# Optimization experiments

Hardware: AMD Instinct MI355X
Metric: run time of the kernel (lower is better)

Reference implementation:

```python
import jax, jax.numpy as jnp
import numpy as np

P = 2          # number of additive secret shares (2-party)
B = 2          # batch
S = 1024       # seq_len
D = 1024       # hidden_size
H = 16         # num_attention_heads
HD = D // H    # attention_head_size = 64
MASK_VAL = -10000.0


def setup_inputs() -> dict:
    key = jax.random.key(0)
    ks = jax.random.split(key, 6)
    w_scale = 0.02
    return {
        "hidden_shares": jax.random.normal(ks[0], (P, B, S, D), jnp.float32),
        "attention_mask": jnp.ones((B, S), jnp.float32),
        "wq": jax.random.normal(ks[1], (D, D), jnp.float32) * w_scale,
        "bq": jnp.zeros((D,), jnp.float32),
        "wk": jax.random.normal(ks[2], (D, D), jnp.float32) * w_scale,
        "bk": jnp.zeros((D,), jnp.float32),
        "wv": jax.random.normal(ks[3], (D, D), jnp.float32) * w_scale,
        "bv": jnp.zeros((D,), jnp.float32),
        "wo": jax.random.normal(ks[4], (D, D), jnp.float32) * w_scale,
        "bo": jnp.zeros((D,), jnp.float32),
    }


def reference(hidden_shares, attention_mask, wq, bq, wk, bk, wv, bv, wo, bo):
    """Secret-shared multi-head attention. Values are carried as P additive
    shares (leading axis); interactive protocol ops (matmul, softmax) are
    modeled as reconstruct -> compute -> reshare with fresh correlated masks,
    which is exactly the plaintext semantics the MPC protocol realizes."""
    scale = np.float32(1.0 / np.sqrt(HD))
    base = jax.random.key(42)  # protocol PRG for resharing masks

    def recon(x):  # [P, ...] -> [...]
        return x.sum(0)

    def reshare(v, tag):  # value -> P additive shares summing to v
        m = jax.random.normal(jax.random.fold_in(base, tag), v.shape, v.dtype) * 0.1
        return jnp.stack([v - m, m])

    def secure_linear(x_sh, w, b, tag):  # torch Linear: x @ w.T + b
        return reshare(recon(x_sh) @ w.T + b, tag)

    def split_heads(x_sh):  # [P,B,S,D] -> [P,B,H,S,HD] (per-share reshape/permute)
        return x_sh.reshape(P, B, S, H, HD).transpose(0, 1, 3, 2, 4)

    q = split_heads(secure_linear(hidden_shares, wq, bq, 0))
    k = split_heads(secure_linear(hidden_shares, wk, bk, 1))
    v = split_heads(secure_linear(hidden_shares, wv, bv, 2))

    # secure QK^T (matmul via reconstruct/reshare), then public scalar scale per-share
    scores = reshare(jnp.einsum('bhsd,bhtd->bhst', recon(q), recon(k)), 3) * scale

    # additive mask, shared, then share-wise secure_add
    additive = (1.0 - attention_mask)[:, None, None, :] * MASK_VAL  # [B,1,1,S]
    scores = scores + reshare(additive, 4)

    probs = reshare(jax.nn.softmax(recon(scores), axis=-1), 5)
    ctx = reshare(jnp.einsum('bhst,bhtd->bhsd', recon(probs), recon(v)), 6)

    # transpose back from scores: [P,B,H,S,HD] -> [P,B,S,D]
    ctx = ctx.transpose(0, 1, 3, 2, 4).reshape(P, B, S, D)

    out = secure_linear(ctx, wo, bo, 7)
    return recon(out)  # reconstructed output [B, S, D]
```

## Files before the change

kernel.cpp:

```cpp
#include <hip/hip_runtime.h>
#include <hip/hip_bf16.h>

#define BB 2
#define SS 1024
#define DD 1024
#define HH 16
#define HDD 64
#define MASK_VAL -10000.0f
#define LOG2E 1.44269504f
#define BSD (BB * SS * DD)
#define NROW (BB * HH * SS)
#define NKV 2

typedef __attribute__((ext_vector_type(8))) short bf16x8;
typedef __attribute__((ext_vector_type(4))) short short4v;
typedef __attribute__((ext_vector_type(4))) float f32x4;
typedef __attribute__((ext_vector_type(16))) float f32x16;
typedef __attribute__((ext_vector_type(4))) unsigned int uint4v;

__device__ __forceinline__ short f2bf(float f) {
    union { float f; unsigned u; } v; v.f = f;
    unsigned r = v.u + 0x7FFFu + ((v.u >> 16) & 1u);
    return (short)(r >> 16);
}
__device__ __forceinline__ float bf2f(short s) {
    union { unsigned u; float f; } v;
    v.u = ((unsigned)(unsigned short)s) << 16;
    return v.f;
}
__device__ __forceinline__ unsigned cvt_pk_bf16(float lo, float hi) {
    unsigned r;
    asm("v_cvt_pk_bf16_f32 %0, %1, %2" : "=v"(r) : "v"(lo), "v"(hi));
    return r;
}
__device__ __forceinline__ float v_exp2(float x) {
    float r;
    asm("v_exp_f32 %0, %1" : "=v"(r) : "v"(x));
    return r;
}
__device__ __forceinline__ void plane32_swap(unsigned& a, unsigned& b) {
#if __has_builtin(__builtin_amdgcn_permlane32_swap)
    auto r = __builtin_amdgcn_permlane32_swap(a, b, false, false);
    a = r[0]; b = r[1];
#else
    unsigned as = (unsigned)__shfl_xor((int)a, 32);
    unsigned bs = (unsigned)__shfl_xor((int)b, 32);
    bool lo = ((threadIdx.x & 63) < 32);
    unsigned na = lo ? a : bs;
    unsigned nb = lo ? as : b;
    a = na; b = nb;
#endif
}

__global__ __launch_bounds__(256) void k_prep(
    const float* __restrict__ h,
    const float* __restrict__ wq, const float* __restrict__ wk,
    const float* __restrict__ wv, const float* __restrict__ wo,
    short* __restrict__ xbf, short* __restrict__ wbf) {
    int id = blockIdx.x;
    if (id < 1024) {
        int i = id * 256 + threadIdx.x;
        const float4* h0 = (const float4*)h;
        const float4* h1 = (const float4*)(h + (size_t)BSD);
        float4 a0 = h0[2 * i], a1 = h0[2 * i + 1];
        float4 b0 = h1[2 * i], b1 = h1[2 * i + 1];
        bf16x8 o;
        o[0] = f2bf(a0.x + b0.x); o[1] = f2bf(a0.y + b0.y);
        o[2] = f2bf(a0.z + b0.z); o[3] = f2bf(a0.w + b0.w);
        o[4] = f2bf(a1.x + b1.x); o[5] = f2bf(a1.y + b1.y);
        o[6] = f2bf(a1.z + b1.z); o[7] = f2bf(a1.w + b1.w);
        ((bf16x8*)xbf)[i] = o;
    } else {
        int zi = (id - 1024) >> 9;
        int i = ((id - 1024) & 511) * 256 + threadIdx.x;
        const float* src = (zi == 0) ? wq : (zi == 1) ? wk : (zi == 2) ? wv : wo;
        short* dst = wbf + (size_t)zi * (DD * DD);
        const float4* s4 = (const float4*)src;
        float4 a0 = s4[2 * i], a1 = s4[2 * i + 1];
        bf16x8 o;
        o[0] = f2bf(a0.x); o[1] = f2bf(a0.y); o[2] = f2bf(a0.z); o[3] = f2bf(a0.w);
        o[4] = f2bf(a1.x); o[5] = f2bf(a1.y); o[6] = f2bf(a1.z); o[7] = f2bf(a1.w);
        ((bf16x8*)dst)[i] = o;
    }
}

#define QBM 128
#define QBN 64
#define QBK 64

__global__ __launch_bounds__(256) void k_gemm_qkv(
    const short* __restrict__ xbf, const short* __restrict__ wbf,
    const float* __restrict__ bq, const float* __restrict__ bk,
    const float* __restrict__ bv,
    short* __restrict__ qb, short* __restrict__ kb, short* __restrict__ vt) {
    __shared__ __align__(16) short As[QBM * QBK];
    __shared__ __align__(16) short Bs[QBN * QBK];
    const int z = blockIdx.z;
    const short* W = wbf + (size_t)z * (DD * DD);
    const float* bias = (z == 0) ? bq : (z == 1) ? bk : bv;
    const int bm = blockIdx.y * QBM;
    const int bn = blockIdx.x * QBN;
    const int tid = threadIdx.x;
    const int lane = tid & 63;
    const int wid = tid >> 6;
    const int wm = wid >> 1;
    const int wn = wid & 1;
    const int lr = lane & 15;
    const int kq = lane >> 4;

    f32x4 acc[4][2];
#pragma unroll
    for (int i = 0; i < 4; ++i)
#pragma unroll
        for (int j = 0; j < 2; ++j) acc[i][j] = (f32x4)0.0f;

    for (int k0 = 0; k0 < DD; k0 += QBK) {
#pragma unroll
        for (int i = 0; i < 4; ++i) {
            int s = i * 256 + tid;
            int r = s >> 3;
            int cs = (s & 7) ^ (r & 7);
            __builtin_amdgcn_global_load_lds(
                (const __attribute__((address_space(1))) unsigned*)(xbf + (size_t)(bm + r) * DD + k0 + (cs << 3)),
                (__attribute__((address_space(3))) unsigned*)&As[s * 8], 16, 0, 0);
        }
#pragma unroll
        for (int i = 0; i < 2; ++i) {
            int s = i * 256 + tid;
            int r = s >> 3;
            int cs = (s & 7) ^ (r & 7);
            __builtin_amdgcn_global_load_lds(
                (const __attribute__((address_space(1))) unsigned*)(W + (size_t)(bn + r) * DD + k0 + (cs << 3)),
                (__attribute__((address_space(3))) unsigned*)&Bs[s * 8], 16, 0, 0);
        }
        __syncthreads();

        bf16x8 af[4][2], bfr[2][2];
#pragma unroll
        for (int f = 0; f < 4; ++f) {
            int row = wm * 64 + f * 16 + lr;
#pragma unroll
            for (int ks = 0; ks < 2; ++ks) {
                int cpos = ((ks << 2) | kq) ^ (row & 7);
                af[f][ks] = *(const bf16x8*)&As[row * QBK + (cpos << 3)];
            }
        }
#pragma unroll
        for (int g = 0; g < 2; ++g) {
            int row = wn * 32 + g * 16 + lr;
#pragma unroll
            for (int ks = 0; ks < 2; ++ks) {
                int cpos = ((ks << 2) | kq) ^ (row & 7);
                bfr[g][ks] = *(const bf16x8*)&Bs[row * QBK + (cpos << 3)];
            }
        }
#pragma unroll
        for (int fm = 0; fm < 4; ++fm)
#pragma unroll
            for (int fn = 0; fn < 2; ++fn)
#pragma unroll
                for (int ks = 0; ks < 2; ++ks)
                    acc[fm][fn] = __builtin_amdgcn_mfma_f32_16x16x32_bf16(
                        af[fm][ks], bfr[fn][ks], acc[fm][fn], 0, 0, 0);
        __syncthreads();
    }

    if (z < 2) {
        short* C = (z == 0) ? qb : kb;
#pragma unroll
        for (int fm = 0; fm < 4; ++fm) {
            int row0 = bm + wm * 64 + fm * 16 + kq * 4;
#pragma unroll
            for (int fn = 0; fn < 2; ++fn) {
                int col = bn + wn * 32 + fn * 16 + lr;
                float bv_ = bias[col];
#pragma unroll
                for (int j = 0; j < 4; ++j)
                    C[(size_t)(row0 + j) * DD + col] = f2bf(acc[fm][fn][j] + bv_);
            }
        }
    } else {
#pragma unroll
        for (int fm = 0; fm < 4; ++fm) {
            int row0 = bm + wm * 64 + fm * 16 + kq * 4;
            int bidx = row0 >> 10, s0 = row0 & 1023;
#pragma unroll
            for (int fn = 0; fn < 2; ++fn) {
                int col = bn + wn * 32 + fn * 16 + lr;
                float bv_ = bias[col];
                size_t addr = ((size_t)(bidx * HH + (col >> 6)) * HDD + (col & 63)) * SS + s0;
                short4v o;
                o.x = f2bf(acc[fm][fn][0] + bv_); o.y = f2bf(acc[fm][fn][1] + bv_);
                o.z = f2bf(acc[fm][fn][2] + bv_); o.w = f2bf(acc[fm][fn][3] + bv_);
                *(short4v*)&vt[addr] = o;
            }
        }
    }
}

#define OM 64
#define ON 64
#define OK 64

__global__ __launch_bounds__(256) void k_gemm_out_fused(
    const short* __restrict__ Op, const float* __restrict__ Mp,
    const float* __restrict__ Lp, const short* __restrict__ W,
    const float* __restrict__ bias, float* __restrict__ C) {
    __shared__ __align__(16) short As[OM * OK];
    __shared__ __align__(16) short Bs[ON * OK];
    const int bm = blockIdx.y * OM;
    const int bn = blockIdx.x * ON;
    const int tid = threadIdx.x;
    const int lane = tid & 63;
    const int wid = tid >> 6;
    const int wm = wid & 1;
    const int wn = wid >> 1;
    const int lr = lane & 15;
    const int kq = lane >> 4;

    f32x4 acc[2][2];
#pragma unroll
    for (int i = 0; i < 2; ++i)
#pragma unroll
        for (int j = 0; j < 2; ++j) acc[i][j] = (f32x4)0.0f;

    for (int k0 = 0; k0 < DD; k0 += OK) {
#pragma unroll
        for (int i = 0; i < 2; ++i) {
            int t2 = i * 256 + tid;
            int br = t2 >> 3;
            int cs = (t2 & 7) ^ (br & 7);
            __builtin_amdgcn_global_load_lds(
                (const __attribute__((address_space(1))) unsigned*)(W + (size_t)(bn + br) * DD + k0 + (cs << 3)),
                (__attribute__((address_space(3))) unsigned*)&Bs[t2 * 8], 16, 0, 0);
        }
        int hh = k0 >> 6;
#pragma unroll
        for (int i = 0; i < 2; ++i) {
            int t2 = i * 256 + tid;
            int ar = t2 >> 3;
            int p = t2 & 7;
            int d0 = (p ^ (ar & 7)) << 3;
            int grow = bm + ar;
            int b = grow >> 10;
            int s = grow & 1023;
            int hrow = ((b * HH + hh) << 10) + s;
            float m1 = Mp[hrow], m2 = Mp[NROW + hrow];
            float l1 = Lp[hrow], l2 = Lp[NROW + hrow];
            float m = fmaxf(m1, m2);
            float a1 = v_exp2(m1 - m), a2 = v_exp2(m2 - m);
            float inv = 1.0f / (l1 * a1 + l2 * a2);
            float c1 = a1 * inv, c2 = a2 * inv;
            bf16x8 o1 = *(const bf16x8*)&Op[(size_t)hrow * HDD + d0];
            bf16x8 o2 = *(const bf16x8*)&Op[((size_t)NROW + hrow) * HDD + d0];
            bf16x8 av;
#pragma unroll
            for (int e = 0; e < 8; ++e)
                av[e] = f2bf(bf2f(o1[e]) * c1 + bf2f(o2[e]) * c2);
            *(bf16x8*)&As[t2 * 8] = av;
        }
        __syncthreads();

        bf16x8 af[2][2], bfr[2][2];
#pragma unroll
        for (int f = 0; f < 2; ++f) {
            int rowa = wm * 32 + f * 16 + lr;
            int rowb = wn * 32 + f * 16 + lr;
#pragma unroll
            for (int ks = 0; ks < 2; ++ks) {
                int ca = (((ks << 2) | kq)) ^ (rowa & 7);
                int cb = (((ks << 2) | kq)) ^ (rowb & 7);
                af[f][ks] = *(const bf16x8*)&As[rowa * OK + (ca << 3)];
                bfr[f][ks] = *(const bf16x8*)&Bs[rowb * OK + (cb << 3)];
            }
        }
#pragma unroll
        for (int fm = 0; fm < 2; ++fm)
#pragma unroll
            for (int fn = 0; fn < 2; ++fn)
#pragma unroll
                for (int ks = 0; ks < 2; ++ks)
                    acc[fm][fn] = __builtin_amdgcn_mfma_f32_16x16x32_bf16(
                        af[fm][ks], bfr[fn][ks], acc[fm][fn], 0, 0, 0);
        __syncthreads();
    }

#pragma unroll
    for (int fm = 0; fm < 2; ++fm) {
        int row0 = bm + wm * 32 + fm * 16 + kq * 4;
#pragma unroll
        for (int fn = 0; fn < 2; ++fn) {
            int col = bn + wn * 32 + fn * 16 + lr;
            float bv_ = bias[col];
#pragma unroll
            for (int j = 0; j < 4; ++j)
                C[(size_t)(row0 + j) * DD + col] = acc[fm][fn][j] + bv_;
        }
    }
}

__global__ __launch_bounds__(256) void k_attn(
    const short* __restrict__ qb, const short* __restrict__ kb,
    const short* __restrict__ vt, const float* __restrict__ mask,
    short* __restrict__ Op, float* __restrict__ Mp, float* __restrict__ Lp) {
    __shared__ __align__(16) short Kls[2][64 * 64];
    __shared__ __align__(16) short Vls[2][64 * 64];

    const int bh = blockIdx.y;
    const int b = bh >> 4;
    const int h = bh & 15;
    const int q0 = blockIdx.x << 7;
    const int kvh = blockIdx.z;
    const int tbase = kvh << 9;
    const int tid = threadIdx.x;
    const int lane = tid & 63;
    const int w = tid >> 6;
    const int ql = lane & 31;
    const int hi = lane >> 5;
    const int rsw = ql & 7;
    const float scale2 = 0.125f * LOG2E;
    const float mval2 = MASK_VAL * LOG2E;

    const short* khead = kb + (size_t)b * SS * DD + h * HDD;
    const short* vhead = vt + (size_t)bh * HDD * SS;
    const float* maskp = mask + b * SS;

    bf16x8 qf0, qf1, qf2, qf3;
    {
        const short* qrow = qb + ((size_t)(b * SS + q0 + w * 32 + ql)) * DD + h * HDD + hi * 8;
        qf0 = *(const bf16x8*)(qrow);
        qf1 = *(const bf16x8*)(qrow + 16);
        qf2 = *(const bf16x8*)(qrow + 32);
        qf3 = *(const bf16x8*)(qrow + 48);
    }

    auto stage = [&](int t0, int bi) {
        const short* kbase = khead + (size_t)t0 * DD;
        const short* vbase = vhead + t0;
#pragma unroll
        for (int i = 0; i < 2; ++i) {
            int t = i * 256 + tid;
            int r = t >> 3;
            int cs = (t & 7) ^ (r & 7);
            __builtin_amdgcn_global_load_lds(
                (const __attribute__((address_space(1))) unsigned*)(kbase + (size_t)r * DD + cs * 8),
                (__attribute__((address_space(3))) unsigned*)&Kls[bi][t * 8], 16, 0, 0);
        }
#pragma unroll
        for (int i = 0; i < 2; ++i) {
            int t = i * 256 + tid;
            int r = t >> 3;
            int cs = (t & 7) ^ (r & 7);
            __builtin_amdgcn_global_load_lds(
                (const __attribute__((address_space(1))) unsigned*)(vbase + (size_t)r * SS + cs * 8),
                (__attribute__((address_space(3))) unsigned*)&Vls[bi][t * 8], 16, 0, 0);
        }
    };

    float m_r = -3.0e38f, l_r = 0.0f;
    f32x16 O0 = (f32x16)0.0f, O1 = (f32x16)0.0f;

    auto body = [&](int t0, int cur, int tail) {
        const short* Kb = &Kls[cur][0];
        const short* Vb = &Vls[cur][0];

        f32x16 s0 = (f32x16)0.0f, s1 = (f32x16)0.0f;
        __builtin_amdgcn_s_setprio(1);
#pragma unroll
        for (int step = 0; step < 4; ++step) {
            int cpos = ((step << 1) | hi) ^ rsw;
            bf16x8 k0 = *(const bf16x8*)&Kb[ql * 64 + (cpos << 3)];
            bf16x8 k1 = *(const bf16x8*)&Kb[(32 + ql) * 64 + (cpos << 3)];
            bf16x8 qf = (step == 0) ? qf0 : (step == 1) ? qf1 : (step == 2) ? qf2 : qf3;
            s0 = __builtin_amdgcn_mfma_f32_32x32x16_bf16(k0, qf, s0, 0, 0, 0);
            s1 = __builtin_amdgcn_mfma_f32_32x32x16_bf16(k1, qf, s1, 0, 0, 0);
        }
        __builtin_amdgcn_s_setprio(0);

#pragma unroll
        for (int g = 0; g < 4; ++g) {
            float4 a4 = *(const float4*)&maskp[t0 + 8 * g + 4 * hi];
            float4 b4 = *(const float4*)&maskp[t0 + 32 + 8 * g + 4 * hi];
            s0[4 * g + 0] = fmaf(s0[4 * g + 0], scale2, (1.0f - a4.x) * mval2);
            s0[4 * g + 1] = fmaf(s0[4 * g + 1], scale2, (1.0f - a4.y) * mval2);
            s0[4 * g + 2] = fmaf(s0[4 * g + 2], scale2, (1.0f - a4.z) * mval2);
            s0[4 * g + 3] = fmaf(s0[4 * g + 3], scale2, (1.0f - a4.w) * mval2);
            s1[4 * g + 0] = fmaf(s1[4 * g + 0], scale2, (1.0f - b4.x) * mval2);
            s1[4 * g + 1] = fmaf(s1[4 * g + 1], scale2, (1.0f - b4.y) * mval2);
            s1[4 * g + 2] = fmaf(s1[4 * g + 2], scale2, (1.0f - b4.z) * mval2);
            s1[4 * g + 3] = fmaf(s1[4 * g + 3], scale2, (1.0f - b4.w) * mval2);
        }

        float mt[16];
#pragma unroll
        for (int r = 0; r < 16; ++r) mt[r] = fmaxf(s0[r], s1[r]);
#pragma unroll
        for (int st = 8; st > 0; st >>= 1)
#pragma unroll
            for (int r = 0; r < 8; ++r)
                if (r < st) mt[r] = fmaxf(mt[r], mt[r + st]);
        float mx = fmaxf(mt[0], __shfl_xor(mt[0], 32));

        bool need = mx > m_r + 8.0f;
        if (__any(need)) {
            float mn = fmaxf(m_r, mx);
            float alpha = v_exp2(m_r - mn);
            m_r = mn;
            l_r *= alpha;
#pragma unroll
            for (int r = 0; r < 16; ++r) {
                int qrow = (r & 3) + 8 * (r >> 2) + 4 * hi;
                float al = __shfl(alpha, qrow, 64);
                O0[r] *= al;
                O1[r] *= al;
            }
        }

        float st0[16];
#pragma unroll
        for (int r = 0; r < 16; ++r) {
            s0[r] = v_exp2(s0[r] - m_r);
            s1[r] = v_exp2(s1[r] - m_r);
            st0[r] = s0[r] + s1[r];
        }
#pragma unroll
        for (int st = 8; st > 0; st >>= 1)
#pragma unroll
            for (int r = 0; r < 8; ++r)
                if (r < st) st0[r] += st0[r + st];
        l_r += st0[0] + __shfl_xor(st0[0], 32);

        unsigned w0 = cvt_pk_bf16(s0[0], s0[1]),  w1 = cvt_pk_bf16(s0[2], s0[3]);
        unsigned w2 = cvt_pk_bf16(s0[4], s0[5]),  w3 = cvt_pk_bf16(s0[6], s0[7]);
        unsigned w4 = cvt_pk_bf16(s0[8], s0[9]),  w5 = cvt_pk_bf16(s0[10], s0[11]);
        unsigned w6 = cvt_pk_bf16(s0[12], s0[13]), w7 = cvt_pk_bf16(s0[14], s0[15]);
        plane32_swap(w0, w2); plane32_swap(w1, w3);
        plane32_swap(w4, w6); plane32_swap(w5, w7);
        uint4v f0 = {w0, w1, w2, w3};
        uint4v f1 = {w4, w5, w6, w7};
        unsigned x0 = cvt_pk_bf16(s1[0], s1[1]),  x1 = cvt_pk_bf16(s1[2], s1[3]);
        unsigned x2 = cvt_pk_bf16(s1[4], s1[5]),  x3 = cvt_pk_bf16(s1[6], s1[7]);
        unsigned x4 = cvt_pk_bf16(s1[8], s1[9]),  x5 = cvt_pk_bf16(s1[10], s1[11]);
        unsigned x6 = cvt_pk_bf16(s1[12], s1[13]), x7 = cvt_pk_bf16(s1[14], s1[15]);
        plane32_swap(x0, x2); plane32_swap(x1, x3);
        plane32_swap(x4, x6); plane32_swap(x5, x7);
        uint4v f2 = {x0, x1, x2, x3};
        uint4v f3 = {x4, x5, x6, x7};

        bf16x8 pf0 = __builtin_bit_cast(bf16x8, f0);
        bf16x8 pf1 = __builtin_bit_cast(bf16x8, f1);
        bf16x8 pf2 = __builtin_bit_cast(bf16x8, f2);
        bf16x8 pf3 = __builtin_bit_cast(bf16x8, f3);

        if (tail) { asm volatile("s_waitcnt vmcnt(0)\n\ts_barrier" ::: "memory"); }
        else      { asm volatile("s_waitcnt vmcnt(4)\n\ts_barrier" ::: "memory"); }

        __builtin_amdgcn_s_setprio(1);
#pragma unroll
        for (int ks = 0; ks < 4; ++ks) {
            int cpos = ((ks << 1) | hi) ^ rsw;
            bf16x8 pf = (ks == 0) ? pf0 : (ks == 1) ? pf1 : (ks == 2) ? pf2 : pf3;
            bf16x8 v0 = *(const bf16x8*)&Vb[ql * 64 + (cpos << 3)];
            bf16x8 v1 = *(const bf16x8*)&Vb[(32 + ql) * 64 + (cpos << 3)];
            O0 = __builtin_amdgcn_mfma_f32_32x32x16_bf16(pf, v0, O0, 0, 0, 0);
            O1 = __builtin_amdgcn_mfma_f32_32x32x16_bf16(pf, v1, O1, 0, 0, 0);
        }
        __builtin_amdgcn_s_setprio(0);
    };

    stage(tbase, 0);
    for (int it = 0; it < 7; ++it) {
        stage(tbase + ((it + 1) << 6), (it + 1) & 1);
        asm volatile("s_waitcnt vmcnt(6)\n\ts_barrier" ::: "memory");
        body(tbase + (it << 6), it & 1, 0);
        asm volatile("s_barrier" ::: "memory");
    }
    asm volatile("s_waitcnt vmcnt(2)\n\ts_barrier" ::: "memory");
    body(tbase + (7 << 6), 1, 1);

    const int rowb = bh * SS + q0 + w * 32;
    short* ob = Op + ((size_t)kvh * NROW + rowb) * HDD;
#pragma unroll
    for (int r = 0; r < 16; ++r) {
        int qrow = (r & 3) + 8 * (r >> 2) + 4 * hi;
        ob[(size_t)qrow * HDD + ql] = f2bf(O0[r]);
        ob[(size_t)qrow * HDD + 32 + ql] = f2bf(O1[r]);
    }
    if (lane < 32) {
        Mp[kvh * NROW + rowb + lane] = m_r;
        Lp[kvh * NROW + rowb + lane] = l_r;
    }
}

extern "C" void kernel_launch(void* const* d_in, const int* in_sizes, int n_in,
                              void* d_out, int out_size, void* d_ws, size_t ws_size,
                              hipStream_t stream) {
    const float* h    = (const float*)d_in[0];
    const float* mask = (const float*)d_in[1];
    const float* wq   = (const float*)d_in[2];
    const float* bq   = (const float*)d_in[3];
    const float* wk   = (const float*)d_in[4];
    const float* bk   = (const float*)d_in[5];
    const float* wv   = (const float*)d_in[6];
    const float* bv   = (const float*)d_in[7];
    const float* wo   = (const float*)d_in[8];
    const float* bo   = (const float*)d_in[9];
    float* out = (float*)d_out;

    char* base = (char*)d_ws;
    short* x_bf  = (short*)base;
    short* w_bf  = (short*)(base + (4u << 20));
    short* q_bf  = (short*)(base + (12u << 20));
    short* k_bf  = (short*)(base + (16u << 20));
    short* v_t   = (short*)(base + (20u << 20));
    short* Op    = (short*)(base + (24u << 20));
    float* Mp    = (float*)(base + (40u << 20));
    float* Lp    = (float*)(base + (40u << 20) + (NKV * NROW * sizeof(float)));

    k_prep<<<3072, 256, 0, stream>>>(h, wq, wk, wv, wo, x_bf, w_bf);

    dim3 gqkv(DD / QBN, BB * SS / QBM, 3);
    k_gemm_qkv<<<gqkv, 256, 0, stream>>>(x_bf, w_bf, bq, bk, bv, q_bf, k_bf, v_t);

    dim3 gattn(SS / 128, BB * HH, NKV);
    k_attn<<<gattn, 256, 0, stream>>>(q_bf, k_bf, v_t, mask, Op, Mp, Lp);

    dim3 gout(DD / ON, BB * SS / OM);
    k_gemm_out_fused<<<gout, 256, 0, stream>>>(Op, Mp, Lp, w_bf + (size_t)3 * DD * DD, bo, out);
}
```

Measured before the change: 73.92 us.

## Double-buffer LDS tiles in QKV and output-projection GEMM kernels

Both the QKV projection GEMM and the fused output-projection GEMM now use two LDS buffers per operand. The next K-tile is issued (async global_load_lds for the weights, plus the softmax-merge of partial attention outputs for A in the output kernel) before the MFMA work on the current tile. The aim is to hide global-load latency behind compute. In exchange it doubles LDS use, which may lower occupancy. The trailing __syncthreads at the end of each iteration is assumed kept, which protects buffer reuse.

Result: no change. 74.81 us (+1.2%).

```diff
diff --git a/kernel.cpp b/kernel.cpp
--- a/kernel.cpp
+++ b/kernel.cpp
@@ -93,8 +93,8 @@
     const float* __restrict__ bq, const float* __restrict__ bk,
     const float* __restrict__ bv,
     short* __restrict__ qb, short* __restrict__ kb, short* __restrict__ vt) {
-    __shared__ __align__(16) short As[QBM * QBK];
-    __shared__ __align__(16) short Bs[QBN * QBK];
+    __shared__ __align__(16) short As[2][QBM * QBK];
+    __shared__ __align__(16) short Bs[2][QBN * QBK];
     const int z = blockIdx.z;
     const short* W = wbf + (size_t)z * (DD * DD);
     const float* bias = (z == 0) ? bq : (z == 1) ? bk : bv;
@@ -114,7 +114,7 @@
 #pragma unroll
         for (int j = 0; j < 2; ++j) acc[i][j] = (f32x4)0.0f;
 
-    for (int k0 = 0; k0 < DD; k0 += QBK) {
+    auto stage = [&](int k0, int bi) {
 #pragma unroll
         for (int i = 0; i < 4; ++i) {
             int s = i * 256 + tid;
@@ -122,7 +122,7 @@
             int cs = (s & 7) ^ (r & 7);
             __builtin_amdgcn_global_load_lds(
                 (const __attribute__((address_space(1))) unsigned*)(xbf + (size_t)(bm + r) * DD + k0 + (cs << 3)),
-                (__attribute__((address_space(3))) unsigned*)&As[s * 8], 16, 0, 0);
+                (__attribute__((address_space(3))) unsigned*)&As[bi][s * 8], 16, 0, 0);
         }
 #pragma unroll
         for (int i = 0; i < 2; ++i) {
@@ -131,9 +131,17 @@
             int cs = (s & 7) ^ (r & 7);
             __builtin_amdgcn_global_load_lds(
                 (const __attribute__((address_space(1))) unsigned*)(W + (size_t)(bn + r) * DD + k0 + (cs << 3)),
-                (__attribute__((address_space(3))) unsigned*)&Bs[s * 8], 16, 0, 0);
-        }
-        __syncthreads();
+                (__attribute__((address_space(3))) unsigned*)&Bs[bi][s * 8], 16, 0, 0);
+        }
+    };
+
+    stage(0, 0);
+    __syncthreads();
+#pragma unroll 1
+    for (int kt = 0; kt < 16; ++kt) {
+        if (kt < 15) stage((kt + 1) * QBK, (kt + 1) & 1);
+        const short* Ab = &As[kt & 1][0];
+        const short* Bb = &Bs[kt & 1][0];
 
         bf16x8 af[4][2], bfr[2][2];
 #pragma unroll
@@ -142,7 +150,7 @@
 #pragma unroll
             for (int ks = 0; ks < 2; ++ks) {
                 int cpos = ((ks << 2) | kq) ^ (row & 7);
-                af[f][ks] = *(const bf16x8*)&As[row * QBK + (cpos << 3)];
+                af[f][ks] = *(const bf16x8*)&Ab[row * QBK + (cpos << 3)];
             }
         }
 #pragma unroll
@@ -151,7 +159,7 @@
 #pragma unroll
             for (int ks = 0; ks < 2; ++ks) {
                 int cpos = ((ks << 2) | kq) ^ (row & 7);
-                bfr[g][ks] = *(const bf16x8*)&Bs[row * QBK + (cpos << 3)];
+                bfr[g][ks] = *(const bf16x8*)&Bb[row * QBK + (cpos << 3)];
             }
         }
 #pragma unroll
@@ -206,8 +214,8 @@
     const short* __restrict__ Op, const float* __restrict__ Mp,
     const float* __restrict__ Lp, const short* __restrict__ W,
     const float* __restrict__ bias, float* __restrict__ C) {
-    __shared__ __align__(16) short As[OM * OK];
-    __shared__ __align__(16) short Bs[ON * OK];
+    __shared__ __align__(16) short As[2][OM * OK];
+    __shared__ __align__(16) short Bs[2][ON * OK];
     const int bm = blockIdx.y * OM;
     const int bn = blockIdx.x * ON;
     const int tid = threadIdx.x;
@@ -224,7 +232,7 @@
 #pragma unroll
         for (int j = 0; j < 2; ++j) acc[i][j] = (f32x4)0.0f;
 
-    for (int k0 = 0; k0 < DD; k0 += OK) {
+    auto stageB = [&](int k0, int bi) {
 #pragma unroll
         for (int i = 0; i < 2; ++i) {
             int t2 = i * 256 + tid;
@@ -232,8 +240,10 @@
             int cs = (t2 & 7) ^ (br & 7);
             __builtin_amdgcn_global_load_lds(
                 (const __attribute__((address_space(1))) unsigned*)(W + (size_t)(bn + br) * DD + k0 + (cs << 3)),
-                (__attribute__((address_space(3))) unsigned*)&Bs[t2 * 8], 16, 0, 0);
-        }
+                (__attribute__((address_space(3))) unsigned*)&Bs[bi][t2 * 8], 16, 0, 0);
+        }
+    };
+    auto mergeA = [&](int k0, int bi) {
         int hh = k0 >> 6;
 #pragma unroll
         for (int i = 0; i < 2; ++i) {
@@ -257,9 +267,18 @@
 #pragma unroll
             for (int e = 0; e < 8; ++e)
                 av[e] = f2bf(bf2f(o1[e]) * c1 + bf2f(o2[e]) * c2);
-            *(bf16x8*)&As[t2 * 8] = av;
-        }
-        __syncthreads();
+            *(bf16x8*)&As[bi][t2 * 8] = av;
+        }
+    };
+
+    stageB(0, 0);
+    mergeA(0, 0);
+    __syncthreads();
+#pragma unroll 1
+    for (int kt = 0; kt < 16; ++kt) {
+        if (kt < 15) { stageB((kt + 1) * OK, (kt + 1) & 1); mergeA((kt + 1) * OK, (kt + 1) & 1); }
+        const short* Ab = &As[kt & 1][0];
+        const short* Bb = &Bs[kt & 1][0];
 
         bf16x8 af[2][2], bfr[2][2];
 #pragma unroll
@@ -270,8 +289,8 @@
             for (int ks = 0; ks < 2; ++ks) {
                 int ca = (((ks << 2) | kq)) ^ (rowa & 7);
                 int cb = (((ks << 2) | kq)) ^ (rowb & 7);
-                af[f][ks] = *(const bf16x8*)&As[rowa * OK + (ca << 3)];
-                bfr[f][ks] = *(const bf16x8*)&Bs[rowb * OK + (cb << 3)];
+                af[f][ks] = *(const bf16x8*)&Ab[rowa * OK + (ca << 3)];
+                bfr[f][ks] = *(const bf16x8*)&Bb[rowb * OK + (cb << 3)];
             }
         }
 #pragma unroll
```

## Software-pipeline attention QK of next tile with softmax/PV of current

Applied to the files above, without the earlier changes.

Splits the attention tile body into a QK^T phase and a softmax+PV phase, then fully unrolls the KV loop so the QK MFMAs for tile i+1 are issued before the softmax and PV of tile i. This lets MFMA work overlap the VALU-heavy softmax. LDS buffering grows from 2 to 4 stages for K and V, which raises LDS use to 64KB per block and may cut occupancy. Two score accumulator pairs increase register pressure.

New measurement: 73.65 us. Within noise of the previous version (-0.4%).

```diff
diff --git a/kernel.cpp b/kernel.cpp
--- a/kernel.cpp
+++ b/kernel.cpp
@@ -303,8 +303,8 @@
     const short* __restrict__ qb, const short* __restrict__ kb,
     const short* __restrict__ vt, const float* __restrict__ mask,
     short* __restrict__ Op, float* __restrict__ Mp, float* __restrict__ Lp) {
-    __shared__ __align__(16) short Kls[2][64 * 64];
-    __shared__ __align__(16) short Vls[2][64 * 64];
+    __shared__ __align__(16) short Kls[4][64 * 64];
+    __shared__ __align__(16) short Vls[4][64 * 64];
 
     const int bh = blockIdx.y;
     const int b = bh >> 4;
@@ -360,11 +360,8 @@
     float m_r = -3.0e38f, l_r = 0.0f;
     f32x16 O0 = (f32x16)0.0f, O1 = (f32x16)0.0f;
 
-    auto body = [&](int t0, int cur, int tail) {
-        const short* Kb = &Kls[cur][0];
-        const short* Vb = &Vls[cur][0];
-
-        f32x16 s0 = (f32x16)0.0f, s1 = (f32x16)0.0f;
+    auto qk = [&](const short* Kb, f32x16& s0, f32x16& s1) {
+        s0 = (f32x16)0.0f; s1 = (f32x16)0.0f;
         __builtin_amdgcn_s_setprio(1);
 #pragma unroll
         for (int step = 0; step < 4; ++step) {
@@ -376,7 +373,9 @@
             s1 = __builtin_amdgcn_mfma_f32_32x32x16_bf16(k1, qf, s1, 0, 0, 0);
         }
         __builtin_amdgcn_s_setprio(0);
-
+    };
+
+    auto finish = [&](int t0, const short* Vb, f32x16& s0, f32x16& s1) {
 #pragma unroll
         for (int g = 0; g < 4; ++g) {
             float4 a4 = *(const float4*)&maskp[t0 + 8 * g + 4 * hi];
@@ -452,9 +451,6 @@
         bf16x8 pf2 = __builtin_bit_cast(bf16x8, f2);
         bf16x8 pf3 = __builtin_bit_cast(bf16x8, f3);
 
-        if (tail) { asm volatile("s_waitcnt vmcnt(0)\n\ts_barrier" ::: "memory"); }
-        else      { asm volatile("s_waitcnt vmcnt(4)\n\ts_barrier" ::: "memory"); }
-
         __builtin_amdgcn_s_setprio(1);
 #pragma unroll
         for (int ks = 0; ks < 4; ++ks) {
@@ -468,15 +464,41 @@
         __builtin_amdgcn_s_setprio(0);
     };
 
+    f32x16 A0, A1, B0, B1;
+
     stage(tbase, 0);
-    for (int it = 0; it < 7; ++it) {
-        stage(tbase + ((it + 1) << 6), (it + 1) & 1);
-        asm volatile("s_waitcnt vmcnt(6)\n\ts_barrier" ::: "memory");
-        body(tbase + (it << 6), it & 1, 0);
-        asm volatile("s_barrier" ::: "memory");
-    }
-    asm volatile("s_waitcnt vmcnt(2)\n\ts_barrier" ::: "memory");
-    body(tbase + (7 << 6), 1, 1);
+    stage(tbase + 64, 1);
+    asm volatile("s_waitcnt vmcnt(4)\n\ts_barrier" ::: "memory");
+    qk(&Kls[0][0], A0, A1);
+
+    stage(tbase + (2 << 6), 2);
+    asm volatile("s_waitcnt vmcnt(4)\n\ts_barrier" ::: "memory");
+    qk(&Kls[1][0], B0, B1);
+    finish(tbase + (0 << 6), &Vls[0][0], A0, A1);
+    stage(tbase + (3 << 6), 3);
+    asm volatile("s_waitcnt vmcnt(4)\n\ts_barrier" ::: "memory");
+    qk(&Kls[2][0], A0, A1);
+    finish(tbase + (1 << 6), &Vls[1][0], B0, B1);
+    stage(tbase + (4 << 6), 0);
+    asm volatile("s_waitcnt vmcnt(4)\n\ts_barrier" ::: "memory");
+    qk(&Kls[3][0], B0, B1);
+    finish(tbase + (2 << 6), &Vls[2][0], A0, A1);
+    stage(tbase + (5 << 6), 1);
+    asm volatile("s_waitcnt vmcnt(4)\n\ts_barrier" ::: "memory");
+    qk(&Kls[0][0], A0, A1);
+    finish(tbase + (3 << 6), &Vls[3][0], B0, B1);
+    stage(tbase + (6 << 6), 2);
+    asm volatile("s_waitcnt vmcnt(4)\n\ts_barrier" ::: "memory");
+    qk(&Kls[1][0], B0, B1);
+    finish(tbase + (4 << 6), &Vls[0][0], A0, A1);
+    stage(tbase + (7 << 6), 3);
+    asm volatile("s_waitcnt vmcnt(4)\n\ts_barrier" ::: "memory");
+    qk(&Kls[2][0], A0, A1);
+    finish(tbase + (5 << 6), &Vls[1][0], B0, B1);
+    asm volatile("s_waitcnt vmcnt(0)\n\ts_barrier" ::: "memory");
+    qk(&Kls[3][0], B0, B1);
+    finish(tbase + (6 << 6), &Vls[2][0], A0, A1);
+    finish(tbase + (7 << 6), &Vls[3][0], B0, B1);
 
     const int rowb = bh * SS + q0 + w * 32;
     short* ob = Op + ((size_t)kvh * NROW + rowb) * HDD;
```

## Merge split-KV attention halves in-block via LDS, emit final context directly

Applied to the files above, without the earlier changes.

The two KV-split halves of attention now run as two 256-thread groups inside one 512-thread block instead of separate blocks. After both finish, the second group writes its partial O, m and l to shared memory, and the first group combines them and writes normalized bf16 context straight into [B,S,D] layout. This removes the global partial-output, max and sum buffers and the combine work in the output GEMM's A-loading, which becomes a plain global-to-LDS copy. In exchange, block count halves, LDS per block doubles (which may reduce occupancy), and the merge step adds extra barriers and serialized epilogue work.

Result: faster. 66.50 us (-10.0%).

```diff
diff --git a/kernel.cpp b/kernel.cpp
--- a/kernel.cpp
+++ b/kernel.cpp
@@ -9,8 +9,6 @@
 #define MASK_VAL -10000.0f
 #define LOG2E 1.44269504f
 #define BSD (BB * SS * DD)
-#define NROW (BB * HH * SS)
-#define NKV 2
 
 typedef __attribute__((ext_vector_type(8))) short bf16x8;
 typedef __attribute__((ext_vector_type(4))) short short4v;
@@ -202,9 +200,8 @@
 #define ON 64
 #define OK 64
 
-__global__ __launch_bounds__(256) void k_gemm_out_fused(
-    const short* __restrict__ Op, const float* __restrict__ Mp,
-    const float* __restrict__ Lp, const short* __restrict__ W,
+__global__ __launch_bounds__(256) void k_gemm_out(
+    const short* __restrict__ A, const short* __restrict__ W,
     const float* __restrict__ bias, float* __restrict__ C) {
     __shared__ __align__(16) short As[OM * OK];
     __shared__ __align__(16) short Bs[ON * OK];
@@ -228,36 +225,20 @@
 #pragma unroll
         for (int i = 0; i < 2; ++i) {
             int t2 = i * 256 + tid;
-            int br = t2 >> 3;
-            int cs = (t2 & 7) ^ (br & 7);
+            int r = t2 >> 3;
+            int cs = (t2 & 7) ^ (r & 7);
             __builtin_amdgcn_global_load_lds(
-                (const __attribute__((address_space(1))) unsigned*)(W + (size_t)(bn + br) * DD + k0 + (cs << 3)),
-                (__attribute__((address_space(3))) unsigned*)&Bs[t2 * 8], 16, 0, 0);
-        }
-        int hh = k0 >> 6;
+                (const __attribute__((address_space(1))) unsigned*)(A + (size_t)(bm + r) * DD + k0 + (cs << 3)),
+                (__attribute__((address_space(3))) unsigned*)&As[t2 * 8], 16, 0, 0);
+        }
 #pragma unroll
         for (int i = 0; i < 2; ++i) {
             int t2 = i * 256 + tid;
-            int ar = t2 >> 3;
-            int p = t2 & 7;
-            int d0 = (p ^ (ar & 7)) << 3;
-            int grow = bm + ar;
-            int b = grow >> 10;
-            int s = grow & 1023;
-            int hrow = ((b * HH + hh) << 10) + s;
-            float m1 = Mp[hrow], m2 = Mp[NROW + hrow];
-            float l1 = Lp[hrow], l2 = Lp[NROW + hrow];
-            float m = fmaxf(m1, m2);
-            float a1 = v_exp2(m1 - m), a2 = v_exp2(m2 - m);
-            float inv = 1.0f / (l1 * a1 + l2 * a2);
-            float c1 = a1 * inv, c2 = a2 * inv;
-            bf16x8 o1 = *(const bf16x8*)&Op[(size_t)hrow * HDD + d0];
-            bf16x8 o2 = *(const bf16x8*)&Op[((size_t)NROW + hrow) * HDD + d0];
-            bf16x8 av;
-#pragma unroll
-            for (int e = 0; e < 8; ++e)
-                av[e] = f2bf(bf2f(o1[e]) * c1 + bf2f(o2[e]) * c2);
-            *(bf16x8*)&As[t2 * 8] = av;
+            int r = t2 >> 3;
+            int cs = (t2 & 7) ^ (r & 7);
+            __builtin_amdgcn_global_load_lds(
+                (const __attribute__((address_space(1))) unsigned*)(W + (size_t)(bn + r) * DD + k0 + (cs << 3)),
+                (__attribute__((address_space(3))) unsigned*)&Bs[t2 * 8], 16, 0, 0);
         }
         __syncthreads();
 
@@ -299,25 +280,26 @@
     }
 }
 
-__global__ __launch_bounds__(256) void k_attn(
+__global__ __launch_bounds__(512) void k_attn(
     const short* __restrict__ qb, const short* __restrict__ kb,
     const short* __restrict__ vt, const float* __restrict__ mask,
-    short* __restrict__ Op, float* __restrict__ Mp, float* __restrict__ Lp) {
-    __shared__ __align__(16) short Kls[2][64 * 64];
-    __shared__ __align__(16) short Vls[2][64 * 64];
+    short* __restrict__ ctx) {
+    __shared__ __align__(16) short Kls[2][2][64 * 64];
+    __shared__ __align__(16) short Vls[2][2][64 * 64];
 
     const int bh = blockIdx.y;
     const int b = bh >> 4;
     const int h = bh & 15;
     const int q0 = blockIdx.x << 7;
-    const int kvh = blockIdx.z;
-    const int tbase = kvh << 9;
     const int tid = threadIdx.x;
+    const int gtid = tid & 255;
+    const int kvh = tid >> 8;
     const int lane = tid & 63;
-    const int w = tid >> 6;
+    const int w4 = (tid >> 6) & 3;
     const int ql = lane & 31;
     const int hi = lane >> 5;
     const int rsw = ql & 7;
+    const int tbase = kvh << 9;
     const float scale2 = 0.125f * LOG2E;
     const float mval2 = MASK_VAL * LOG2E;
 
@@ -327,7 +309,7 @@
 
     bf16x8 qf0, qf1, qf2, qf3;
     {
-        const short* qrow = qb + ((size_t)(b * SS + q0 + w * 32 + ql)) * DD + h * HDD + hi * 8;
+        const short* qrow = qb + ((size_t)(b * SS + q0 + w4 * 32 + ql)) * DD + h * HDD + hi * 8;
         qf0 = *(const bf16x8*)(qrow);
         qf1 = *(const bf16x8*)(qrow + 16);
         qf2 = *(const bf16x8*)(qrow + 32);
@@ -339,21 +321,21 @@
         const short* vbase = vhead + t0;
 #pragma unroll
         for (int i = 0; i < 2; ++i) {
-            int t = i * 256 + tid;
+            int t = i * 256 + gtid;
             int r = t >> 3;
             int cs = (t & 7) ^ (r & 7);
             __builtin_amdgcn_global_load_lds(
                 (const __attribute__((address_space(1))) unsigned*)(kbase + (size_t)r * DD + cs * 8),
-                (__attribute__((address_space(3))) unsigned*)&Kls[bi][t * 8], 16, 0, 0);
+                (__attribute__((address_space(3))) unsigned*)&Kls[kvh][bi][t * 8], 16, 0, 0);
         }
 #pragma unroll
         for (int i = 0; i < 2; ++i) {
-            int t = i * 256 + tid;
+            int t = i * 256 + gtid;
             int r = t >> 3;
             int cs = (t & 7) ^ (r & 7);
             __builtin_amdgcn_global_load_lds(
                 (const __attribute__((address_space(1))) unsigned*)(vbase + (size_t)r * SS + cs * 8),
-                (__attribute__((address_space(3))) unsigned*)&Vls[bi][t * 8], 16, 0, 0);
+                (__attribute__((address_space(3))) unsigned*)&Vls[kvh][bi][t * 8], 16, 0, 0);
         }
     };
 
@@ -361,8 +343,8 @@
     f32x16 O0 = (f32x16)0.0f, O1 = (f32x16)0.0f;
 
     auto body = [&](int t0, int cur, int tail) {
-        const short* Kb = &Kls[cur][0];
-        const short* Vb = &Vls[cur][0];
+        const short* Kb = &Kls[kvh][cur][0];
+        const short* Vb = &Vls[kvh][cur][0];
 
         f32x16 s0 = (f32x16)0.0f, s1 = (f32x16)0.0f;
         __builtin_amdgcn_s_setprio(1);
@@ -432,12 +414,12 @@
 
         unsigned w0 = cvt_pk_bf16(s0[0], s0[1]),  w1 = cvt_pk_bf16(s0[2], s0[3]);
         unsigned w2 = cvt_pk_bf16(s0[4], s0[5]),  w3 = cvt_pk_bf16(s0[6], s0[7]);
-        unsigned w4 = cvt_pk_bf16(s0[8], s0[9]),  w5 = cvt_pk_bf16(s0[10], s0[11]);
+        unsigned w4_ = cvt_pk_bf16(s0[8], s0[9]),  w5 = cvt_pk_bf16(s0[10], s0[11]);
         unsigned w6 = cvt_pk_bf16(s0[12], s0[13]), w7 = cvt_pk_bf16(s0[14], s0[15]);
         plane32_swap(w0, w2); plane32_swap(w1, w3);
-        plane32_swap(w4, w6); plane32_swap(w5, w7);
+        plane32_swap(w4_, w6); plane32_swap(w5, w7);
         uint4v f0 = {w0, w1, w2, w3};
-        uint4v f1 = {w4, w5, w6, w7};
+        uint4v f1 = {w4_, w5, w6, w7};
         unsigned x0 = cvt_pk_bf16(s1[0], s1[1]),  x1 = cvt_pk_bf16(s1[2], s1[3]);
         unsigned x2 = cvt_pk_bf16(s1[4], s1[5]),  x3 = cvt_pk_bf16(s1[6], s1[7]);
         unsigned x4 = cvt_pk_bf16(s1[8], s1[9]),  x5 = cvt_pk_bf16(s1[10], s1[11]);
@@ -478,17 +460,42 @@
     asm volatile("s_waitcnt vmcnt(2)\n\ts_barrier" ::: "memory");
     body(tbase + (7 << 6), 1, 1);
 
-    const int rowb = bh * SS + q0 + w * 32;
-    short* ob = Op + ((size_t)kvh * NROW + rowb) * HDD;
-#pragma unroll
-    for (int r = 0; r < 16; ++r) {
-        int qrow = (r & 3) + 8 * (r >> 2) + 4 * hi;
-        ob[(size_t)qrow * HDD + ql] = f2bf(O0[r]);
-        ob[(size_t)qrow * HDD + 32 + ql] = f2bf(O1[r]);
-    }
-    if (lane < 32) {
-        Mp[kvh * NROW + rowb + lane] = m_r;
-        Lp[kvh * NROW + rowb + lane] = l_r;
+    __syncthreads();
+    float* osh = (float*)&Kls[0][0][0];
+    float* mlsh = (float*)&Vls[0][0][0];
+    if (kvh == 1) {
+        float* obuf = osh + w4 * 2048;
+#pragma unroll
+        for (int r = 0; r < 16; ++r) {
+            int qrow = (r & 3) + 8 * (r >> 2) + 4 * hi;
+            obuf[qrow * 64 + ql] = O0[r];
+            obuf[qrow * 64 + 32 + ql] = O1[r];
+        }
+        if (lane < 32) {
+            mlsh[w4 * 64 + ql] = m_r;
+            mlsh[w4 * 64 + 32 + ql] = l_r;
+        }
+    }
+    __syncthreads();
+    if (kvh == 0) {
+        float* obuf = osh + w4 * 2048;
+        float m2 = mlsh[w4 * 64 + ql];
+        float l2 = mlsh[w4 * 64 + 32 + ql];
+        float m = fmaxf(m_r, m2);
+        float a1 = v_exp2(m_r - m), a2 = v_exp2(m2 - m);
+        float inv = 1.0f / (l_r * a1 + l2 * a2);
+        float c1 = a1 * inv, c2 = a2 * inv;
+        short* cb = ctx + ((size_t)(b * SS + q0 + w4 * 32)) * DD + h * HDD;
+#pragma unroll
+        for (int r = 0; r < 16; ++r) {
+            int qrow = (r & 3) + 8 * (r >> 2) + 4 * hi;
+            float cc1 = __shfl(c1, qrow, 64);
+            float cc2 = __shfl(c2, qrow, 64);
+            float ob0 = obuf[qrow * 64 + ql];
+            float ob1 = obuf[qrow * 64 + 32 + ql];
+            cb[(size_t)qrow * DD + ql]      = f2bf(O0[r] * cc1 + ob0 * cc2);
+            cb[(size_t)qrow * DD + 32 + ql] = f2bf(O1[r] * cc1 + ob1 * cc2);
+        }
     }
 }
 
@@ -513,18 +520,16 @@
     short* q_bf  = (short*)(base + (12u << 20));
     short* k_bf  = (short*)(base + (16u << 20));
     short* v_t   = (short*)(base + (20u << 20));
-    short* Op    = (short*)(base + (24u << 20));
-    float* Mp    = (float*)(base + (40u << 20));
-    float* Lp    = (float*)(base + (40u << 20) + (NKV * NROW * sizeof(float)));
+    short* ctxbf = (short*)(base + (24u << 20));
 
     k_prep<<<3072, 256, 0, stream>>>(h, wq, wk, wv, wo, x_bf, w_bf);
 
     dim3 gqkv(DD / QBN, BB * SS / QBM, 3);
     k_gemm_qkv<<<gqkv, 256, 0, stream>>>(x_bf, w_bf, bq, bk, bv, q_bf, k_bf, v_t);
 
-    dim3 gattn(SS / 128, BB * HH, NKV);
-    k_attn<<<gattn, 256, 0, stream>>>(q_bf, k_bf, v_t, mask, Op, Mp, Lp);
+    dim3 gattn(SS / 128, BB * HH);
+    k_attn<<<gattn, 512, 0, stream>>>(q_bf, k_bf, v_t, mask, ctxbf);
 
     dim3 gout(DD / ON, BB * SS / OM);
-    k_gemm_out_fused<<<gout, 256, 0, stream>>>(Op, Mp, Lp, w_bf + (size_t)3 * DD * DD, bo, out);
-}
+    k_gemm_out<<<gout, 256, 0, stream>>>(ctxbf, w_bf + (size_t)3 * DD * DD, bo, out);
+}
```
